# Optimization experiments

Hardware: AMD Instinct MI355X
Metric: run time of the kernel (lower is better)

Reference implementation:

```python
import jax, jax.numpy as jnp
import numpy as np

K = 3
LAMBDA_AMP = 0.1
N_NODES = 100000
N_EDGES = 1600000
D_FEAT = 50


def _proximal_l21(x, lambda_):
    # rowwise L2,1 shrinkage: scale each row by max(||row||-lambda,0)/||row||
    row_norm = jnp.linalg.norm(x, axis=1)  # [N]
    score = jnp.maximum(row_norm - lambda_, 0.0)
    score = jnp.where(row_norm > 0, score / jnp.where(row_norm > 0, row_norm, 1.0), score)
    return score[:, None] * x


def setup_inputs() -> dict:
    key = jax.random.key(0)
    k1, k2, k3, k4 = jax.random.split(key, 4)
    feat = jax.random.normal(k1, (N_NODES, D_FEAT), dtype=jnp.float32)
    edge_weight = jax.random.uniform(k2, (N_EDGES,), dtype=jnp.float32)
    src = jax.random.randint(k3, (N_EDGES,), 0, N_NODES, dtype=jnp.int32)
    dst = jax.random.randint(k4, (N_EDGES,), 0, N_NODES, dtype=jnp.int32)
    return {"feat": feat, "edge_weight": edge_weight, "src": src, "dst": dst}


def reference(feat, edge_weight, src, dst):
    n = feat.shape[0]
    # add self-loops (add_self_loop=True), self-loop weight = 1
    loop = jnp.arange(n, dtype=src.dtype)
    src_f = jnp.concatenate([src, loop])
    dst_f = jnp.concatenate([dst, loop])
    ew = jnp.concatenate([edge_weight, jnp.ones((n,), dtype=edge_weight.dtype)])

    # norm='both': w_ji = ew / (sqrt(out_deg(j)) * sqrt(in_deg(i))), weighted degrees
    out_deg = jax.ops.segment_sum(ew, src_f, num_segments=n)
    in_deg = jax.ops.segment_sum(ew, dst_f, num_segments=n)
    inv_sqrt_out = jnp.where(out_deg > 0, out_deg, 1.0) ** -0.5 * (out_deg > 0)
    inv_sqrt_in = jnp.where(in_deg > 0, in_deg, 1.0) ** -0.5 * (in_deg > 0)
    w = ew * inv_sqrt_out[src_f] * inv_sqrt_in[dst_f]  # [E+N]

    lam = LAMBDA_AMP
    gamma = 1.0 / (2.0 * (1.0 - lam))
    hh = feat
    x = feat
    for _ in range(K):
        # compute_LX: x - A_norm x  (u_mul_e + sum == SpMM over edges)
        agg = jax.ops.segment_sum(x[src_f] * w[:, None], dst_f, num_segments=n)
        lx = x - agg
        y = x - gamma * 2.0 * (1.0 - lam) * lx
        x = hh + _proximal_l21(y - hh, gamma * lam)
    return x
```

## Files before the change

### kernel.cpp

```cpp
#include <hip/hip_runtime.h>
#include <hip/hip_bf16.h>
#include <hip/hip_fp16.h>

#define D 50
#define PADH 64
#define GLAM 0.05555555555555555f
#define SCAN_B 1024
#define FIXS 8388608.0f
#define INV_FIXS (1.0f / 8388608.0f)
#define EPB 8192
#define B2T 512
#define BSH 9
#define BMSK 511u
#define BT 512
#define MAXB 256

typedef unsigned long long u64;

__global__ void k_b1p(const int* __restrict__ src, const int* __restrict__ dst,
                      int* __restrict__ mat, const float* __restrict__ feat,
                      __half* __restrict__ xp, int e, int nblk, int nbuk, int n) {
    if ((int)blockIdx.x < nblk) {
        __shared__ unsigned hd[MAXB], hs[MAXB];
        for (int j = threadIdx.x; j < nbuk; j += blockDim.x) { hd[j] = 0; hs[j] = 0; }
        __syncthreads();
        int base = blockIdx.x * EPB;
        int end = base + EPB; if (end > e) end = e;
        for (int i = base + threadIdx.x; i < end; i += blockDim.x) {
            int t = __builtin_nontemporal_load(dst + i);
            int s = __builtin_nontemporal_load(src + i);
            atomicAdd(&hd[t >> BSH], 1u);
            atomicAdd(&hs[s >> BSH], 1u);
        }
        __syncthreads();
        for (int j = threadIdx.x; j < nbuk; j += blockDim.x) {
            mat[j * nblk + blockIdx.x] = (int)hd[j];
            mat[(nbuk + j) * nblk + blockIdx.x] = (int)hs[j];
        }
    } else {
        int i = ((int)blockIdx.x - nblk) * (int)blockDim.x + (int)threadIdx.x;
        if (i < n * PADH) {
            int node = i >> 6, col = i & 63;
            xp[i] = (col < D) ? __float2half_rn(feat[node * D + col]) : __half(0.0f);
        }
    }
}

__global__ void k_scan1(const int* __restrict__ cnt, int* __restrict__ out,
                        int* __restrict__ bsum, int n) {
    __shared__ int s[SCAN_B];
    int i = blockIdx.x * SCAN_B + threadIdx.x;
    int v = (i < n) ? cnt[i] : 0;
    s[threadIdx.x] = v; __syncthreads();
    for (int off = 1; off < SCAN_B; off <<= 1) {
        int t = (threadIdx.x >= (unsigned)off) ? s[threadIdx.x - off] : 0;
        __syncthreads();
        s[threadIdx.x] += t; __syncthreads();
    }
    if (i < n) out[i] = s[threadIdx.x] - v;
    if (threadIdx.x == SCAN_B - 1) bsum[blockIdx.x] = s[threadIdx.x];
}

__global__ void k_scan2(int* __restrict__ bsum, int nb) {
    __shared__ int s[SCAN_B];
    int v = (threadIdx.x < (unsigned)nb) ? bsum[threadIdx.x] : 0;
    s[threadIdx.x] = v; __syncthreads();
    for (int off = 1; off < SCAN_B; off <<= 1) {
        int t = (threadIdx.x >= (unsigned)off) ? s[threadIdx.x - off] : 0;
        __syncthreads();
        s[threadIdx.x] += t; __syncthreads();
    }
    if (threadIdx.x < (unsigned)nb) bsum[threadIdx.x] = s[threadIdx.x] - v;
}

__global__ void k_scan3(int* __restrict__ out, const int* __restrict__ bsum, int n) {
    int i = blockIdx.x * SCAN_B + threadIdx.x;
    if (i < n) out[i] += bsum[blockIdx.x];
}

__global__ void k_b2(const float* __restrict__ ew, const int* __restrict__ src,
                     const int* __restrict__ dst, const int* __restrict__ msc,
                     u64* __restrict__ bind, unsigned* __restrict__ bins,
                     int e, int nblk, int nbuk) {
    __shared__ unsigned cd[MAXB], cs[MAXB];
    __shared__ unsigned ld[MAXB], ls[MAXB];
    __shared__ int gbd[MAXB], gbs[MAXB];
    __shared__ u64 sd[EPB];
    __shared__ unsigned ss[EPB];
    __shared__ unsigned char bdd[EPB], bds[EPB];
    int tid = threadIdx.x;
    for (int j = tid; j < MAXB; j += blockDim.x) { cd[j] = 0; cs[j] = 0; }
    __syncthreads();
    int base = blockIdx.x * EPB;
    int end = base + EPB; if (end > e) end = e;
    int m = end - base;

    for (int i = base + tid; i < end; i += blockDim.x) {
        atomicAdd(&cd[(unsigned)__builtin_nontemporal_load(dst + i) >> BSH], 1u);
        atomicAdd(&cs[(unsigned)__builtin_nontemporal_load(src + i) >> BSH], 1u);
    }
    __syncthreads();

    unsigned vd = 0, vs = 0;
    if (tid < MAXB) { vd = cd[tid]; vs = cs[tid]; ld[tid] = vd; ls[tid] = vs; }
    __syncthreads();
    for (int off = 1; off < MAXB; off <<= 1) {
        unsigned td = 0, ts = 0;
        if (tid < MAXB && tid >= off) { td = ld[tid - off]; ts = ls[tid - off]; }
        __syncthreads();
        if (tid < MAXB) { ld[tid] += td; ls[tid] += ts; }
        __syncthreads();
    }
    if (tid < MAXB) {
        ld[tid] -= vd; ls[tid] -= vs;
        cd[tid] = ld[tid]; cs[tid] = ls[tid];
        if (tid < nbuk) {
            gbd[tid] = msc[tid * nblk + blockIdx.x];
            gbs[tid] = msc[(nbuk + tid) * nblk + blockIdx.x] - e;
        }
    }
    __syncthreads();

    for (int i = base + tid; i < end; i += blockDim.x) {
        float w = __builtin_nontemporal_load(ew + i);
        int s = __builtin_nontemporal_load(src + i);
        int t = __builtin_nontemporal_load(dst + i);
        unsigned wfix = (unsigned)(w * FIXS + 0.5f);
        if (wfix > 0x7FFFFFu) wfix = 0x7FFFFFu;
        unsigned tb = (unsigned)t >> BSH, sb = (unsigned)s >> BSH;
        unsigned pd = atomicAdd(&cd[tb], 1u);
        sd[pd] = ((u64)__float_as_uint(w) << 32)
               | ((unsigned)s << BSH) | (unsigned)(t & BMSK);
        bdd[pd] = (unsigned char)tb;
        unsigned ps = atomicAdd(&cs[sb], 1u);
        ss[ps] = (wfix << BSH) | (unsigned)(s & BMSK);
        bds[ps] = (unsigned char)sb;
    }
    __syncthreads();

    for (int p = tid; p < m; p += blockDim.x) {
        unsigned jd = bdd[p];
        bind[gbd[jd] + (int)(p - ld[jd])] = sd[p];
        unsigned js = bds[p];
        bins[gbs[js] + (int)(p - ls[js])] = ss[p];
    }
}

__global__ void k_srcdeg(const unsigned* __restrict__ bins, const int* __restrict__ msc,
                         float* __restrict__ iso, int n, int nblk, int nbuk, int e) {
    __shared__ unsigned wl[BT];
    wl[threadIdx.x] = 0;
    __syncthreads();
    int b = blockIdx.x;
    int start = msc[(nbuk + b) * nblk] - e;
    int end = (b + 1 < nbuk) ? (msc[(nbuk + b + 1) * nblk] - e) : e;
    for (int i = start + threadIdx.x; i < end; i += blockDim.x) {
        unsigned r = bins[i];
        atomicAdd(&wl[r & BMSK], r >> BSH);
    }
    __syncthreads();
    int node = b * BT + threadIdx.x;
    if (node < n)
        iso[node] = rsqrtf(1.0f + (float)wl[threadIdx.x] * INV_FIXS);
}

__global__ void k_dstfill(const u64* __restrict__ bind, const int* __restrict__ msc,
                          const float* __restrict__ iso, float* __restrict__ isi,
                          int* __restrict__ cnt, int* __restrict__ rowptr,
                          u64* __restrict__ pe, int n, int nblk, int nbuk, int e) {
    __shared__ unsigned cl[BT], wl[BT], cur[BT];
    __shared__ int sc[BT];
    __shared__ float isL[BT];
    cl[threadIdx.x] = 0; wl[threadIdx.x] = 0;
    __syncthreads();
    int b = blockIdx.x;
    int start = msc[b * nblk];
    int end = (b + 1 < nbuk) ? msc[(b + 1) * nblk] : e;

    for (int i = start + threadIdx.x; i < end; i += blockDim.x) {
        u64 r = bind[i];
        unsigned loc = (unsigned)r & BMSK;
        float w = __uint_as_float((unsigned)(r >> 32));
        unsigned wfix = (unsigned)(w * FIXS + 0.5f);
        if (wfix > 0x7FFFFFu) wfix = 0x7FFFFFu;
        atomicAdd(&cl[loc], 1u);
        atomicAdd(&wl[loc], wfix);
    }
    __syncthreads();

    int myc = (int)cl[threadIdx.x];
    sc[threadIdx.x] = myc;
    __syncthreads();
    for (int off = 1; off < BT; off <<= 1) {
        int t = (threadIdx.x >= (unsigned)off) ? sc[threadIdx.x - off] : 0;
        __syncthreads();
        sc[threadIdx.x] += t;
        __syncthreads();
    }
    int lrp = start + sc[threadIdx.x] - myc;

    float myisi = rsqrtf(1.0f + (float)wl[threadIdx.x] * INV_FIXS);
    isL[threadIdx.x] = myisi;
    cur[threadIdx.x] = (unsigned)lrp;

    int node = b * BT + threadIdx.x;
    if (node < n) {
        isi[node] = myisi;
        cnt[node] = myc;
        rowptr[node] = lrp;
    }
    __syncthreads();

    for (int i = start + threadIdx.x; i < end; i += blockDim.x) {
        u64 r = bind[i];
        unsigned lo = (unsigned)r;
        unsigned tloc = lo & BMSK;
        unsigned s = lo >> BSH;
        float w = __uint_as_float((unsigned)(r >> 32));
        float wv = w * iso[s] * isL[tloc];
        unsigned pos = atomicAdd(&cur[tloc], 1u);
        pe[pos] = (u64)s | ((u64)__float_as_uint(wv) << 32);
    }
}

__device__ __forceinline__ void acc_edge(const uint4& u, float w,
                                         float& a0, float& a1, float& a2, float& a3,
                                         float& a4, float& a5, float& a6, float& a7) {
    const __half2* hp = (const __half2*)&u;
    float2 f0 = __half22float2(hp[0]);
    float2 f1 = __half22float2(hp[1]);
    float2 f2 = __half22float2(hp[2]);
    float2 f3 = __half22float2(hp[3]);
    a0 = fmaf(w, f0.x, a0); a1 = fmaf(w, f0.y, a1);
    a2 = fmaf(w, f1.x, a2); a3 = fmaf(w, f1.y, a3);
    a4 = fmaf(w, f2.x, a4); a5 = fmaf(w, f2.y, a5);
    a6 = fmaf(w, f3.x, a6); a7 = fmaf(w, f3.y, a7);
}

__global__ void k_iter(const int* __restrict__ rowptr, const int* __restrict__ cnt,
                       const u64* __restrict__ pe, const __half* __restrict__ xin,
                       const __half* __restrict__ xpF, const float* __restrict__ iso,
                       const float* __restrict__ isi, __half* __restrict__ hout,
                       float* __restrict__ fout, int n, int final_iter) {
    int lane = threadIdx.x & 63;
    int c    = lane & 7;
    int waveId = (blockIdx.x * blockDim.x + threadIdx.x) >> 6;
    int node = waveId * 8 + (lane >> 3);
    if (node >= n) return;

    float a0 = 0.f, a1 = 0.f, a2 = 0.f, a3 = 0.f;
    float a4 = 0.f, a5 = 0.f, a6 = 0.f, a7 = 0.f;

    int beg = rowptr[node], m = cnt[node];

    int j = 0;
    for (; j + 4 <= m; j += 4) {
        u64 p0 = pe[beg + j];
        u64 p1 = pe[beg + j + 1];
        u64 p2 = pe[beg + j + 2];
        u64 p3 = pe[beg + j + 3];
        unsigned s0 = (unsigned)p0; float w0 = __uint_as_float((unsigned)(p0 >> 32));
        unsigned s1 = (unsigned)p1; float w1 = __uint_as_float((unsigned)(p1 >> 32));
        unsigned s2 = (unsigned)p2; float w2 = __uint_as_float((unsigned)(p2 >> 32));
        unsigned s3 = (unsigned)p3; float w3 = __uint_as_float((unsigned)(p3 >> 32));
        uint4 u0 = *(const uint4*)(xin + ((size_t)s0 << 6) + (c << 3));
        uint4 u1 = *(const uint4*)(xin + ((size_t)s1 << 6) + (c << 3));
        uint4 u2 = *(const uint4*)(xin + ((size_t)s2 << 6) + (c << 3));
        uint4 u3 = *(const uint4*)(xin + ((size_t)s3 << 6) + (c << 3));
        acc_edge(u0, w0, a0, a1, a2, a3, a4, a5, a6, a7);
        acc_edge(u1, w1, a0, a1, a2, a3, a4, a5, a6, a7);
        acc_edge(u2, w2, a0, a1, a2, a3, a4, a5, a6, a7);
        acc_edge(u3, w3, a0, a1, a2, a3, a4, a5, a6, a7);
    }
    for (; j < m; ++j) {
        u64 p0 = pe[beg + j];
        unsigned s0 = (unsigned)p0;
        float    w0 = __uint_as_float((unsigned)(p0 >> 32));
        uint4 u0 = *(const uint4*)(xin + ((size_t)s0 << 6) + (c << 3));
        acc_edge(u0, w0, a0, a1, a2, a3, a4, a5, a6, a7);
    }

    float selfw = iso[node] * isi[node];
    {
        uint4 u = *(const uint4*)(xin + ((size_t)node << 6) + (c << 3));
        acc_edge(u, selfw, a0, a1, a2, a3, a4, a5, a6, a7);
    }

    float f[8];
    {
        uint4 u = *(const uint4*)(xpF + ((size_t)node << 6) + (c << 3));
        const __half2* hp = (const __half2*)&u;
        float2 f0 = __half22float2(hp[0]);
        float2 f1 = __half22float2(hp[1]);
        float2 f2 = __half22float2(hp[2]);
        float2 f3 = __half22float2(hp[3]);
        f[0] = f0.x; f[1] = f0.y; f[2] = f1.x; f[3] = f1.y;
        f[4] = f2.x; f[5] = f2.y; f[6] = f3.x; f[7] = f3.y;
    }

    float d0 = a0 - f[0], d1 = a1 - f[1], d2 = a2 - f[2], d3 = a3 - f[3];
    float d4 = a4 - f[4], d5 = a5 - f[5], d6 = a6 - f[6], d7 = a7 - f[7];

    float ssum = d0*d0 + d1*d1 + d2*d2 + d3*d3 + d4*d4 + d5*d5 + d6*d6 + d7*d7;
    ssum += __shfl_xor(ssum, 1, 64);
    ssum += __shfl_xor(ssum, 2, 64);
    ssum += __shfl_xor(ssum, 4, 64);
    float norm = sqrtf(ssum);
    float sc = (norm > 0.0f) ? fmaxf(norm - GLAM, 0.0f) / norm : 0.0f;

    float o0 = f[0] + sc * d0, o1 = f[1] + sc * d1;
    float o2 = f[2] + sc * d2, o3 = f[3] + sc * d3;
    float o4 = f[4] + sc * d4, o5 = f[5] + sc * d5;
    float o6 = f[6] + sc * d6, o7 = f[7] + sc * d7;
    if (!final_iter) {
        __half2 h0 = __float22half2_rn(make_float2(o0, o1));
        __half2 h1 = __float22half2_rn(make_float2(o2, o3));
        __half2 h2 = __float22half2_rn(make_float2(o4, o5));
        __half2 h3 = __float22half2_rn(make_float2(o6, o7));
        uint4 u;
        u.x = *(unsigned*)&h0; u.y = *(unsigned*)&h1;
        u.z = *(unsigned*)&h2; u.w = *(unsigned*)&h3;
        *(uint4*)(hout + ((size_t)node << 6) + (c << 3)) = u;
    } else {
        float o[8] = {o0, o1, o2, o3, o4, o5, o6, o7};
        int fb = c << 3;
        #pragma unroll
        for (int k = 0; k < 4; ++k) {
            int ff = fb + (k << 1);
            if (ff + 1 < D) {
                float2 v; v.x = o[k * 2]; v.y = o[k * 2 + 1];
                *(float2*)(fout + (size_t)node * D + ff) = v;
            }
        }
    }
}

extern "C" void kernel_launch(void* const* d_in, const int* in_sizes, int n_in,
                              void* d_out, int out_size, void* d_ws, size_t ws_size,
                              hipStream_t stream) {
    const float* feat = (const float*)d_in[0];
    const float* ew   = (const float*)d_in[1];
    const int* src = (const int*)d_in[2];
    const int* dst = (const int*)d_in[3];

    const int nd = in_sizes[0];
    const int n  = nd / D;
    const int e  = in_sizes[1];
    const int np = n * PADH;

    const int nbuk = (n + BT - 1) / BT;
    const int nblk = (e + EPB - 1) / EPB;
    const int nm   = 2 * nbuk * nblk;

    __half*   xpF    = (__half*)d_ws;
    __half*   xpA    = xpF + np;
    __half*   xpB    = xpA + np;
    u64*      bind   = (u64*)(xpB + np);
    u64*      pe     = bind + e;
    unsigned* bins   = (unsigned*)(pe + e);
    int*      mat    = (int*)(bins + e);
    int*      msc    = mat + nm;
    float*    isi    = (float*)(msc + nm);
    float*    iso    = isi + n;
    int*      cnt    = (int*)(iso + n);
    int*      rowptr = cnt + n;
    int*      bsum   = rowptr + n;
    float*    out    = (float*)d_out;

    const int B = 256;
    const int gP  = (np + B2T - 1) / B2T;
    const int NBm = (nm + SCAN_B - 1) / SCAN_B;

    k_b1p<<<nblk + gP, B2T, 0, stream>>>(src, dst, mat, feat, xpF, e, nblk, nbuk, n);
    k_scan1<<<NBm, SCAN_B, 0, stream>>>(mat, msc, bsum, nm);
    k_scan2<<<1, SCAN_B, 0, stream>>>(bsum, NBm);
    k_scan3<<<NBm, SCAN_B, 0, stream>>>(msc, bsum, nm);
    k_b2<<<nblk, B2T, 0, stream>>>(ew, src, dst, msc, bind, bins, e, nblk, nbuk);
    k_srcdeg<<<nbuk, BT, 0, stream>>>(bins, msc, iso, n, nblk, nbuk, e);
    k_dstfill<<<nbuk, BT, 0, stream>>>(bind, msc, iso, isi, cnt, rowptr, pe, n, nblk, nbuk, e);

    const int nodesPerBlock = (B / 64) * 8;
    const int iterGrid = (n + nodesPerBlock - 1) / nodesPerBlock;

    k_iter<<<iterGrid, B, 0, stream>>>(rowptr, cnt, pe, xpF, xpF, iso, isi, xpA, out, n, 0);
    k_iter<<<iterGrid, B, 0, stream>>>(rowptr, cnt, pe, xpA, xpF, iso, isi, xpB, out, n, 0);
    k_iter<<<iterGrid, B, 0, stream>>>(rowptr, cnt, pe, xpB, xpF, iso, isi, xpA, out, n, 1);
}
```

Measured before the change: 266.5 us.

## Pack edge records into 32-bit source+quantized weight and stage bucket records in LDS

Edge records used by the SpMM iterations shrink from 64-bit (source index plus float weight) to 32-bit, holding a 17-bit source index and a 15-bit fixed-point normalized weight. This halves edge-list traffic in each of the three aggregation passes and in the fill write. The fill kernel also caches its bucket's records in shared memory so the second pass does not re-read global memory, falling back to the old path when a bucket is too large. The risks are weight quantization error, a source-index limit of 2^17 nodes, and the large LDS allocation lowering occupancy.

```diff
diff --git a/kernel.cpp b/kernel.cpp
--- a/kernel.cpp
+++ b/kernel.cpp
@@ -8,12 +8,15 @@
 #define SCAN_B 1024
 #define FIXS 8388608.0f
 #define INV_FIXS (1.0f / 8388608.0f)
+#define WSC 32768.0f
+#define INV_WSC (1.0f / 32768.0f)
 #define EPB 8192
 #define B2T 512
 #define BSH 9
 #define BMSK 511u
 #define BT 512
 #define MAXB 256
+#define MAXRUN 12288
 
 typedef unsigned long long u64;
 
@@ -167,7 +170,8 @@
 __global__ void k_dstfill(const u64* __restrict__ bind, const int* __restrict__ msc,
                           const float* __restrict__ iso, float* __restrict__ isi,
                           int* __restrict__ cnt, int* __restrict__ rowptr,
-                          u64* __restrict__ pe, int n, int nblk, int nbuk, int e) {
+                          unsigned* __restrict__ pe, int n, int nblk, int nbuk, int e) {
+    __shared__ u64 recs[MAXRUN];
     __shared__ unsigned cl[BT], wl[BT], cur[BT];
     __shared__ int sc[BT];
     __shared__ float isL[BT];
@@ -176,15 +180,30 @@
     int b = blockIdx.x;
     int start = msc[b * nblk];
     int end = (b + 1 < nbuk) ? msc[(b + 1) * nblk] : e;
-
-    for (int i = start + threadIdx.x; i < end; i += blockDim.x) {
-        u64 r = bind[i];
-        unsigned loc = (unsigned)r & BMSK;
-        float w = __uint_as_float((unsigned)(r >> 32));
-        unsigned wfix = (unsigned)(w * FIXS + 0.5f);
-        if (wfix > 0x7FFFFFu) wfix = 0x7FFFFFu;
-        atomicAdd(&cl[loc], 1u);
-        atomicAdd(&wl[loc], wfix);
+    int run = end - start;
+    bool fast = (run <= MAXRUN);
+
+    if (fast) {
+        for (int i = threadIdx.x; i < run; i += blockDim.x) {
+            u64 r = bind[start + i];
+            recs[i] = r;
+            unsigned loc = (unsigned)r & BMSK;
+            float w = __uint_as_float((unsigned)(r >> 32));
+            unsigned wfix = (unsigned)(w * FIXS + 0.5f);
+            if (wfix > 0x7FFFFFu) wfix = 0x7FFFFFu;
+            atomicAdd(&cl[loc], 1u);
+            atomicAdd(&wl[loc], wfix);
+        }
+    } else {
+        for (int i = start + threadIdx.x; i < end; i += blockDim.x) {
+            u64 r = bind[i];
+            unsigned loc = (unsigned)r & BMSK;
+            float w = __uint_as_float((unsigned)(r >> 32));
+            unsigned wfix = (unsigned)(w * FIXS + 0.5f);
+            if (wfix > 0x7FFFFFu) wfix = 0x7FFFFFu;
+            atomicAdd(&cl[loc], 1u);
+            atomicAdd(&wl[loc], wfix);
+        }
     }
     __syncthreads();
 
@@ -211,15 +230,32 @@
     }
     __syncthreads();
 
-    for (int i = start + threadIdx.x; i < end; i += blockDim.x) {
-        u64 r = bind[i];
-        unsigned lo = (unsigned)r;
-        unsigned tloc = lo & BMSK;
-        unsigned s = lo >> BSH;
-        float w = __uint_as_float((unsigned)(r >> 32));
-        float wv = w * iso[s] * isL[tloc];
-        unsigned pos = atomicAdd(&cur[tloc], 1u);
-        pe[pos] = (u64)s | ((u64)__float_as_uint(wv) << 32);
+    if (fast) {
+        for (int i = threadIdx.x; i < run; i += blockDim.x) {
+            u64 r = recs[i];
+            unsigned lo = (unsigned)r;
+            unsigned tloc = lo & BMSK;
+            unsigned s = lo >> BSH;
+            float w = __uint_as_float((unsigned)(r >> 32));
+            float wv = w * iso[s] * isL[tloc];
+            unsigned wq = (unsigned)(wv * WSC + 0.5f);
+            if (wq > 32767u) wq = 32767u;
+            unsigned pos = atomicAdd(&cur[tloc], 1u);
+            pe[pos] = (s << 15) | wq;
+        }
+    } else {
+        for (int i = start + threadIdx.x; i < end; i += blockDim.x) {
+            u64 r = bind[i];
+            unsigned lo = (unsigned)r;
+            unsigned tloc = lo & BMSK;
+            unsigned s = lo >> BSH;
+            float w = __uint_as_float((unsigned)(r >> 32));
+            float wv = w * iso[s] * isL[tloc];
+            unsigned wq = (unsigned)(wv * WSC + 0.5f);
+            if (wq > 32767u) wq = 32767u;
+            unsigned pos = atomicAdd(&cur[tloc], 1u);
+            pe[pos] = (s << 15) | wq;
+        }
     }
 }
 
@@ -238,7 +274,7 @@
 }
 
 __global__ void k_iter(const int* __restrict__ rowptr, const int* __restrict__ cnt,
-                       const u64* __restrict__ pe, const __half* __restrict__ xin,
+                       const unsigned* __restrict__ pe, const __half* __restrict__ xin,
                        const __half* __restrict__ xpF, const float* __restrict__ iso,
                        const float* __restrict__ isi, __half* __restrict__ hout,
                        float* __restrict__ fout, int n, int final_iter) {
@@ -255,14 +291,14 @@
 
     int j = 0;
     for (; j + 4 <= m; j += 4) {
-        u64 p0 = pe[beg + j];
-        u64 p1 = pe[beg + j + 1];
-        u64 p2 = pe[beg + j + 2];
-        u64 p3 = pe[beg + j + 3];
-        unsigned s0 = (unsigned)p0; float w0 = __uint_as_float((unsigned)(p0 >> 32));
-        unsigned s1 = (unsigned)p1; float w1 = __uint_as_float((unsigned)(p1 >> 32));
-        unsigned s2 = (unsigned)p2; float w2 = __uint_as_float((unsigned)(p2 >> 32));
-        unsigned s3 = (unsigned)p3; float w3 = __uint_as_float((unsigned)(p3 >> 32));
+        unsigned p0 = pe[beg + j];
+        unsigned p1 = pe[beg + j + 1];
+        unsigned p2 = pe[beg + j + 2];
+        unsigned p3 = pe[beg + j + 3];
+        unsigned s0 = p0 >> 15; float w0 = (float)(p0 & 32767u) * INV_WSC;
+        unsigned s1 = p1 >> 15; float w1 = (float)(p1 & 32767u) * INV_WSC;
+        unsigned s2 = p2 >> 15; float w2 = (float)(p2 & 32767u) * INV_WSC;
+        unsigned s3 = p3 >> 15; float w3 = (float)(p3 & 32767u) * INV_WSC;
         uint4 u0 = *(const uint4*)(xin + ((size_t)s0 << 6) + (c << 3));
         uint4 u1 = *(const uint4*)(xin + ((size_t)s1 << 6) + (c << 3));
         uint4 u2 = *(const uint4*)(xin + ((size_t)s2 << 6) + (c << 3));
@@ -273,9 +309,9 @@
         acc_edge(u3, w3, a0, a1, a2, a3, a4, a5, a6, a7);
     }
     for (; j < m; ++j) {
-        u64 p0 = pe[beg + j];
-        unsigned s0 = (unsigned)p0;
-        float    w0 = __uint_as_float((unsigned)(p0 >> 32));
+        unsigned p0 = pe[beg + j];
+        unsigned s0 = p0 >> 15;
+        float    w0 = (float)(p0 & 32767u) * INV_WSC;
         uint4 u0 = *(const uint4*)(xin + ((size_t)s0 << 6) + (c << 3));
         acc_edge(u0, w0, a0, a1, a2, a3, a4, a5, a6, a7);
     }
@@ -356,8 +392,8 @@
     __half*   xpA    = xpF + np;
     __half*   xpB    = xpA + np;
     u64*      bind   = (u64*)(xpB + np);
-    u64*      pe     = bind + e;
-    unsigned* bins   = (unsigned*)(pe + e);
+    unsigned* pe     = (unsigned*)(bind + e);
+    unsigned* bins   = pe + e;
     int*      mat    = (int*)(bins + e);
     int*      msc    = mat + nm;
     float*    isi    = (float*)(msc + nm);
```

After: 258.7 us. 1.03x faster.
